# Optimization experiments

Measured on AMD Instinct MI355X. Metric: run time of the kernel, lower is better.

Reference implementation:

```python
import jax, jax.numpy as jnp
import numpy as np

C = 128          # hidden channels
N = 40000        # nodes
E = 640000       # edges (avg degree 16)
G = 64           # graphs in batch
STEPS = (5, 4, 3, 2, 1)  # num_layers of each GatedGraphConv


def setup_inputs() -> dict:
    key = jax.random.key(0)
    ks = jax.random.split(key, 9)
    x = jax.random.normal(ks[0], (N, C), jnp.float32)
    edge_index = jax.random.randint(ks[1], (2, E), 0, N, dtype=jnp.int64)
    edge_weights = jax.random.uniform(ks[2], (E,), jnp.float32)
    batch = jnp.sort(jax.random.randint(ks[3], (N,), 0, G, dtype=jnp.int64))
    s = 1.0 / np.sqrt(C)
    # conv_w[k, i] = per-step propagation weight of conv k (unused steps padded)
    conv_w = jax.random.uniform(ks[4], (5, 5, C, C), jnp.float32, -s, s)
    gru_wih = jax.random.uniform(ks[5], (5, 3 * C, C), jnp.float32, -s, s)
    gru_whh = jax.random.uniform(ks[6], (5, 3 * C, C), jnp.float32, -s, s)
    gru_bih = jax.random.uniform(ks[7], (5, 3 * C), jnp.float32, -s, s)
    gru_bhh = jax.random.uniform(ks[8], (5, 3 * C), jnp.float32, -s, s)
    gn_w = jnp.ones((4, C), jnp.float32)
    gn_b = jnp.zeros((4, C), jnp.float32)
    gn_ms = jnp.ones((4, C), jnp.float32)  # GraphNorm mean_scale
    return {"x": x, "edge_weights": edge_weights, "conv_w": conv_w,
            "gru_wih": gru_wih, "gru_whh": gru_whh, "gru_bih": gru_bih,
            "gru_bhh": gru_bhh, "gn_w": gn_w, "gn_b": gn_b, "gn_ms": gn_ms,
            "edge_index": edge_index, "batch": batch}


def _gru(m, h, wih, whh, bih, bhh):
    gi = m @ wih.T + bih
    gh = h @ whh.T + bhh
    ir, iz, inew = jnp.split(gi, 3, axis=-1)
    hr, hz, hn = jnp.split(gh, 3, axis=-1)
    r = jax.nn.sigmoid(ir + hr)
    z = jax.nn.sigmoid(iz + hz)
    n = jnp.tanh(inew + r * hn)
    return (1.0 - z) * n + z * h


def _ggc(x, W, wih, whh, bih, bhh, src, dst, ew, steps):
    # PyG GatedGraphConv: m = x W_i; aggregate sum of ew * m[src] at dst; GRU update.
    for i in range(steps):
        m = x @ W[i]
        msg = m[src]
        if ew is not None:
            msg = msg * ew[:, None]
        agg = jax.ops.segment_sum(msg, dst, num_segments=x.shape[0])
        x = _gru(agg, x, wih, whh, bih, bhh)
    return x


def _graph_norm(x, w, b, ms, eps=1e-5):
    # called with batch=None -> normalize over all nodes as one graph
    mean = jnp.mean(x, axis=0)
    xc = x - ms * mean
    var = jnp.mean(xc * xc, axis=0)
    return w * xc / jnp.sqrt(var + eps) + b


def reference(x, edge_weights, conv_w, gru_wih, gru_whh, gru_bih, gru_bhh,
              gn_w, gn_b, gn_ms, edge_index, batch):
    src, dst = edge_index[0], edge_index[1]
    lrelu = jax.nn.leaky_relu
    o = _ggc(x, conv_w[0], gru_wih[0], gru_whh[0], gru_bih[0], gru_bhh[0], src, dst, edge_weights, STEPS[0])
    o = _graph_norm(o, gn_w[0], gn_b[0], gn_ms[0])
    o = lrelu(o)
    o = _ggc(o, conv_w[1], gru_wih[1], gru_whh[1], gru_bih[1], gru_bhh[1], src, dst, edge_weights, STEPS[1])
    o = lrelu(o)
    o = _graph_norm(o, gn_w[1], gn_b[1], gn_ms[1])
    o = _ggc(o, conv_w[2], gru_wih[2], gru_whh[2], gru_bih[2], gru_bhh[2], src, dst, edge_weights, STEPS[2])
    o = lrelu(o)
    o = _graph_norm(o, gn_w[2], gn_b[2], gn_ms[2])
    o = _ggc(o, conv_w[3], gru_wih[3], gru_whh[3], gru_bih[3], gru_bhh[3], src, dst, edge_weights, STEPS[3])
    o = lrelu(o)
    o = _graph_norm(o, gn_w[3], gn_b[3], gn_ms[3])
    o = _ggc(o, conv_w[4], gru_wih[4], gru_whh[4], gru_bih[4], gru_bhh[4], src, dst, None, STEPS[4])
    o = lrelu(o)
    return jax.ops.segment_sum(o, batch, num_segments=G)
```

## Files before the change

### kernel.cpp

```cpp
#include <hip/hip_runtime.h>
#include <hip/hip_bf16.h>

#define NN 40000
#define EE 640000
#define CCH 128
#define GG 64

typedef __attribute__((ext_vector_type(8))) short short8;
typedef __attribute__((ext_vector_type(4))) float f32x4;

__device__ __forceinline__ float lrelu01(float v){ return v > 0.f ? v : 0.01f*v; }
__device__ __forceinline__ float sigm(float v){ return 1.f/(1.f + __expf(-v)); }
__device__ __forceinline__ float tanh_f(float v){
  v = fminf(fmaxf(v, -15.f), 15.f);
  const float t = __expf(2.f*v);
  return (t - 1.f)/(t + 1.f);
}
__device__ __forceinline__ unsigned short f2bf(float f){
  union { float f; unsigned int u; } v; v.f = f;
  const unsigned int r = v.u + 0x7FFFu + ((v.u >> 16) & 1u);
  return (unsigned short)(r >> 16);
}
__device__ __forceinline__ float bf2f(unsigned short h){
  union { unsigned int u; float f; } v; v.u = ((unsigned int)h) << 16;
  return v.f;
}
__device__ __forceinline__ void split2v(const float4 a, const float4 b, short8& hi, short8& lo){
  const float v[8] = {a.x,a.y,a.z,a.w,b.x,b.y,b.z,b.w};
#pragma unroll
  for (int i=0;i<8;++i){
    const unsigned short h = f2bf(v[i]);
    hi[i] = (short)h;
    lo[i] = (short)f2bf(v[i] - bf2f(h));
  }
}
__device__ __forceinline__ float LDF(const void* p, int f32, size_t i){
  return f32 ? ((const float*)p)[i] : bf2f(((const unsigned short*)p)[i]);
}
__device__ __forceinline__ int LDI(const void* p, int i64, size_t i){
  return i64 ? (int)((const long long*)p)[i] : ((const int*)p)[i];
}

__global__ __launch_bounds__(256) void k_detect(const unsigned short* __restrict__ xh,
                                                const unsigned int* __restrict__ ei,
                                                int* __restrict__ flags){
  __shared__ int s1[256], s2[256];
  const int t = threadIdx.x;
  int c1 = 0, c2 = 0;
  for (int i=0;i<8;++i){
    const unsigned short w = xh[t*8 + i];
    const int e = (w >> 7) & 0xFF;
    if (e < 100 || e > 140) c1++;
    const unsigned int o = ei[(t*8 + i)*2 + 1];
    if (o) c2++;
  }
  s1[t]=c1; s2[t]=c2; __syncthreads();
  for (int off=128; off; off>>=1){ if (t<off){ s1[t]+=s1[t+off]; s2[t]+=s2[t+off]; } __syncthreads(); }
  if (t==0){
    flags[0] = (s1[0] > 64) ? 1 : 0;
    flags[1] = (s2[0] < 16) ? 1 : 0;
  }
}

__global__ __launch_bounds__(256) void k_hist(const void* __restrict__ eidx, const int* __restrict__ flags,
                                              int* __restrict__ deg){
  const int e = blockIdx.x*256 + threadIdx.x;
  if (e >= EE) return;
  atomicAdd(&deg[LDI(eidx, flags[1], (size_t)EE + e)], 1);
}

__global__ __launch_bounds__(256) void k_scan1(const int* __restrict__ deg, int* __restrict__ bsum){
  __shared__ int s[256];
  const int t = threadIdx.x;
  const int i = blockIdx.x*256 + t;
  s[t] = (i < NN) ? deg[i] : 0;
  __syncthreads();
  for (int off=128; off; off>>=1){ if (t<off) s[t]+=s[t+off]; __syncthreads(); }
  if (t==0) bsum[blockIdx.x] = s[0];
}

__global__ __launch_bounds__(256) void k_scan2(const int* __restrict__ bsum, int* __restrict__ boff,
                                               int* __restrict__ roff){
  __shared__ int s[256];
  const int t = threadIdx.x;
  const int v = (t < 157) ? bsum[t] : 0;
  s[t] = v; __syncthreads();
  for (int off=1; off<256; off<<=1){
    const int u = (t>=off) ? s[t-off] : 0;
    __syncthreads(); s[t] += u; __syncthreads();
  }
  if (t < 157) boff[t] = s[t] - v;
  if (t == 0) roff[NN] = EE;
}

__global__ __launch_bounds__(256) void k_scan3(const int* __restrict__ deg, const int* __restrict__ boff,
                                               int* __restrict__ roff, int* __restrict__ pos){
  __shared__ int s[256];
  const int t = threadIdx.x;
  const int i = blockIdx.x*256 + t;
  const int v = (i < NN) ? deg[i] : 0;
  s[t] = v; __syncthreads();
  for (int off=1; off<256; off<<=1){
    const int u = (t>=off) ? s[t-off] : 0;
    __syncthreads(); s[t] += u; __syncthreads();
  }
  if (i < NN){
    const int ex = boff[blockIdx.x] + s[t] - v;
    roff[i] = ex; pos[i] = ex;
  }
}

__global__ __launch_bounds__(256) void k_scatter(const void* __restrict__ eidx, const void* __restrict__ ew,
                                                 const int* __restrict__ flags,
                                                 int* __restrict__ pos, int* __restrict__ es, float* __restrict__ ewt){
  const int e = blockIdx.x*256 + threadIdx.x;
  if (e >= EE) return;
  const int i64 = flags[1];
  const int d = LDI(eidx, i64, (size_t)EE + e);
  const int p = atomicAdd(&pos[d], 1);
  es[p] = LDI(eidx, i64, e);
  ewt[p] = LDF(ew, flags[0], e);
}

__global__ __launch_bounds__(256) void k_x2f(const void* __restrict__ xin, const int* __restrict__ flags,
                                             float* __restrict__ xf){
  const int i = blockIdx.x*256 + threadIdx.x;
  if (i < NN*CCH) xf[i] = LDF(xin, flags[0], i);
}

__global__ __launch_bounds__(256) void k_batcvt(const void* __restrict__ batch, const int* __restrict__ flags,
                                                int* __restrict__ bat32){
  const int i = blockIdx.x*256 + threadIdx.x;
  if (i < NN) bat32[i] = LDI(batch, flags[1], i);
}

__global__ __launch_bounds__(256) void k_wcvt_bf(const void* __restrict__ w, const int* __restrict__ flags,
                                                 const size_t off, unsigned short* __restrict__ o, const int n){
  const int i = blockIdx.x*256 + threadIdx.x;
  if (i < n) o[i] = f2bf(LDF(w, flags[0], off + i));
}

__global__ __launch_bounds__(256) void k_mkWc(const void* __restrict__ cw, const void* __restrict__ wih,
                                              const int* __restrict__ flags,
                                              unsigned short* __restrict__ wcH, unsigned short* __restrict__ wcL){
  __shared__ unsigned short sW[128*128];
  __shared__ unsigned short sI[32*136];
  const int tid = threadIdx.x;
  const int t = blockIdx.x / 12, tile = blockIdx.x % 12;
  int L=0, s=t;
  if (t>=14){L=4;s=t-14;} else if(t>=12){L=3;s=t-12;} else if(t>=9){L=2;s=t-9;} else if(t>=5){L=1;s=t-5;}
  const int f32 = flags[0];
  const size_t woff = (size_t)(L*5+s)*16384;
  const size_t ioff = (size_t)L*49152 + (size_t)tile*32*128;
  for (int u=tid; u<16384; u+=256) sW[u] = f2bf(LDF(cw, f32, woff + u));
  for (int u=tid; u<4096; u+=256){
    const int r = u>>7, jj = u&127;
    sI[r*136 + jj] = f2bf(LDF(wih, f32, ioff + r*128 + jj));
  }
  __syncthreads();
  const int cl = tid & 31;
  const int kb = (tid>>5)*16;
  for (int k=kb; k<kb+16; ++k){
    float acc = 0.f;
#pragma unroll 4
    for (int j8=0; j8<16; ++j8){
      const short8 a = *(const short8*)(sW + k*128 + j8*8);
      const short8 b = *(const short8*)(sI + cl*136 + j8*8);
#pragma unroll
      for (int q=0;q<8;++q) acc += bf2f((unsigned short)a[q]) * bf2f((unsigned short)b[q]);
    }
    const unsigned short h = f2bf(acc);
    const unsigned short l = f2bf(acc - bf2f(h));
    const size_t oidx = (size_t)t*49152 + (size_t)(tile*32 + cl)*128 + k;
    wcH[oidx] = h; wcL[oidx] = l;
  }
}

__global__ __launch_bounds__(256) void k_agg(const float* __restrict__ m, const int* __restrict__ roff,
                                             const int* __restrict__ es, const float* __restrict__ ewt,
                                             float* __restrict__ agg, const int useW){
  const int node = (blockIdx.x*256 + threadIdx.x) >> 6;
  if (node >= NN) return;
  const int lane = threadIdx.x & 63;
  const int h = lane >> 5, j = lane & 31;
  const int beg = roff[node], end = roff[node+1];
  float ax=0.f, ay=0.f, az=0.f, aw=0.f;
  int e = beg + h;
  for (; e + 2 < end; e += 4){
    const int s0 = es[e], s1 = es[e+2];
    const float w0 = useW ? ewt[e] : 1.f;
    const float w1 = useW ? ewt[e+2] : 1.f;
    const float4 v0 = *(const float4*)(m + (size_t)s0*CCH + j*4);
    const float4 v1 = *(const float4*)(m + (size_t)s1*CCH + j*4);
    ax += w0*v0.x + w1*v1.x; ay += w0*v0.y + w1*v1.y;
    az += w0*v0.z + w1*v1.z; aw += w0*v0.w + w1*v1.w;
  }
  if (e < end){
    const int s0 = es[e];
    const float w0 = useW ? ewt[e] : 1.f;
    const float4 v0 = *(const float4*)(m + (size_t)s0*CCH + j*4);
    ax += w0*v0.x; ay += w0*v0.y; az += w0*v0.z; aw += w0*v0.w;
  }
  ax += __shfl_xor(ax, 32); ay += __shfl_xor(ay, 32);
  az += __shfl_xor(az, 32); aw += __shfl_xor(aw, 32);
  if (h == 0){
    float4 ov; ov.x=ax; ov.y=ay; ov.z=az; ov.w=aw;
    *(float4*)(agg + (size_t)node*CCH + j*4) = ov;
  }
}

__global__ __launch_bounds__(256) void k_gru(const float* __restrict__ xg,
                                             const float* __restrict__ xc,
                                             float* __restrict__ xn,
                                             const unsigned short* __restrict__ wcH,
                                             const unsigned short* __restrict__ wcL,
                                             const unsigned short* __restrict__ whB,
                                             const void* __restrict__ bih, const void* __restrict__ bhh,
                                             const size_t boff, const int* __restrict__ flags){
  __shared__ unsigned short s_w[6*32*128];
  const int tid = threadIdx.x;
  const int wv = tid >> 6;
  const int lane = tid & 63;
  const int quad = lane >> 4;
  const int ln = lane & 15;
  const int bi_ = blockIdx.x >> 2, j = blockIdx.x & 3;
  const int m0 = bi_*64 + wv*16;
  const int f32 = flags[0];
  float4 ra[8], rx[8];
  {
    const float* pa = xg + (size_t)(m0 + ln)*CCH + quad*8;
    const float* px = xc + (size_t)(m0 + ln)*CCH + quad*8;
#pragma unroll
    for (int kk=0;kk<4;++kk){
      ra[kk*2]   = *(const float4*)(pa + kk*32);
      ra[kk*2+1] = *(const float4*)(pa + kk*32 + 4);
      rx[kk*2]   = *(const float4*)(px + kk*32);
      rx[kk*2+1] = *(const float4*)(px + kk*32 + 4);
    }
  }
  for (int u = tid; u < 3072; u += 256){
    const int chunk = u >> 9;
    const int rem = u & 511;
    const int c = rem >> 4, p = rem & 15;
    const int gate = (chunk < 3) ? chunk : chunk - 3;
    const unsigned short* src = ((chunk < 3) ? wcH : wcL)
        + ((size_t)(gate*CCH + j*32 + c)*CCH + p*8);
    *(short8*)(s_w + chunk*4096 + c*128 + ((p ^ (c & 15))*8)) = *(const short8*)src;
  }
  short8 fah[4], fal[4], fxh[4], fxl[4];
#pragma unroll
  for (int kk=0;kk<4;++kk){
    split2v(ra[kk*2], ra[kk*2+1], fah[kk], fal[kk]);
    split2v(rx[kk*2], rx[kk*2+1], fxh[kk], fxl[kk]);
  }
  __syncthreads();
  f32x4 acci[2][3];
#pragma unroll
  for (int hf=0; hf<2; ++hf){
    const int c_local = hf*16 + ln;
#pragma unroll
    for (int g=0;g<3;++g) acci[hf][g] = (f32x4){0.f,0.f,0.f,0.f};
#pragma unroll
    for (int kk=0;kk<4;++kk){
      const int sw = ((kk*4+quad) ^ (c_local & 15))*8;
#pragma unroll
      for (int g=0;g<3;++g){
        const short8 bh_ = *(const short8*)(s_w + g*4096     + c_local*128 + sw);
        const short8 bl_ = *(const short8*)(s_w + (3+g)*4096 + c_local*128 + sw);
        acci[hf][g] = __builtin_amdgcn_mfma_f32_16x16x32_bf16(fah[kk], bh_, acci[hf][g], 0, 0, 0);
        acci[hf][g] = __builtin_amdgcn_mfma_f32_16x16x32_bf16(fal[kk], bh_, acci[hf][g], 0, 0, 0);
        acci[hf][g] = __builtin_amdgcn_mfma_f32_16x16x32_bf16(fah[kk], bl_, acci[hf][g], 0, 0, 0);
      }
    }
  }
  __syncthreads();
  for (int u = tid; u < 1536; u += 256){
    const int chunk = u >> 9;
    const int rem = u & 511;
    const int c = rem >> 4, p = rem & 15;
    const unsigned short* src = whB + ((size_t)(chunk*CCH + j*32 + c)*CCH + p*8);
    *(short8*)(s_w + chunk*4096 + c*128 + ((p ^ (c & 15))*8)) = *(const short8*)src;
  }
  __syncthreads();
#pragma unroll 1
  for (int hf=0; hf<2; ++hf){
    const int c_local = hf*16 + ln;
    f32x4 acch[3];
#pragma unroll
    for (int g=0;g<3;++g) acch[g] = (f32x4){0.f,0.f,0.f,0.f};
#pragma unroll
    for (int kk=0;kk<4;++kk){
      const int sw = ((kk*4+quad) ^ (c_local & 15))*8;
#pragma unroll
      for (int g=0;g<3;++g){
        const short8 bh_ = *(const short8*)(s_w + g*4096 + c_local*128 + sw);
        acch[g] = __builtin_amdgcn_mfma_f32_16x16x32_bf16(fxh[kk], bh_, acch[g], 0, 0, 0);
        acch[g] = __builtin_amdgcn_mfma_f32_16x16x32_bf16(fxl[kk], bh_, acch[g], 0, 0, 0);
      }
    }
    const int col = j*32 + c_local;
    float bi[3], bh[3];
#pragma unroll
    for (int g=0;g<3;++g){
      bi[g] = LDF(bih, f32, boff + g*CCH + col);
      bh[g] = LDF(bhh, f32, boff + g*CCH + col);
    }
#pragma unroll
    for (int r=0;r<4;++r){
      const int row = m0 + quad*4 + r;
      const size_t idx = (size_t)row*CCH + col;
      const float h = xc[idx];
      const float rr = sigm(acci[hf][0][r] + acch[0][r] + bi[0] + bh[0]);
      const float zz = sigm(acci[hf][1][r] + acch[1][r] + bi[1] + bh[1]);
      const float nv = tanh_f(acci[hf][2][r] + bi[2] + rr*(acch[2][r] + bh[2]));
      xn[idx] = (1.f - zz)*nv + zz*h;
    }
  }
}

__global__ __launch_bounds__(256) void k_gn_stats(const float* __restrict__ x, float* __restrict__ accum, const int pre){
  const int tid = threadIdx.x;
  const int ch = tid & 127;
  const int half = tid >> 7;
  const int node0 = blockIdx.x * 128;
  float s = 0.f, s2 = 0.f;
  for (int r = half; r < 128; r += 2){
    const int n = node0 + r;
    if (n >= NN) break;
    float v = x[(size_t)n*CCH + ch];
    if (pre) v = lrelu01(v);
    s += v; s2 += v*v;
  }
  __shared__ float buf[256];
  buf[tid] = s; __syncthreads();
  if (tid < 128) atomicAdd(&accum[ch], buf[tid] + buf[tid+128]);
  __syncthreads();
  buf[tid] = s2; __syncthreads();
  if (tid < 128) atomicAdd(&accum[128+ch], buf[tid] + buf[tid+128]);
}

__global__ void k_gn_final(const float* __restrict__ accum, const void* __restrict__ gw,
                           const void* __restrict__ gb, const void* __restrict__ gms,
                           const size_t off, const int* __restrict__ flags, float* __restrict__ par){
  const int j = threadIdx.x;
  const int f32 = flags[0];
  const float inv = 1.f/(float)NN;
  const float mean = accum[j]*inv;
  const float m2 = accum[128+j]*inv;
  const float ms = LDF(gms, f32, off + j);
  const float var = m2 - 2.f*ms*mean*mean + ms*ms*mean*mean;
  const float sc = LDF(gw, f32, off + j) / sqrtf(var + 1e-5f);
  par[j] = sc;
  par[128+j] = LDF(gb, f32, off + j) - sc*ms*mean;
}

__global__ __launch_bounds__(256) void k_gn_apply(float* __restrict__ xf, const float* __restrict__ par, const int mode){
  const int i = blockIdx.x*256 + threadIdx.x;
#pragma unroll
  for (int r=0;r<8;++r){
    const int idx = i + r*640000;
    float v = xf[idx];
    const int ch = idx & 127;
    if (mode == 1) v = lrelu01(v);
    v = par[ch]*v + par[128+ch];
    if (mode == 0) v = lrelu01(v);
    xf[idx] = v;
  }
}

__global__ __launch_bounds__(256) void k_final(const float* __restrict__ x, const int* __restrict__ bat,
                                               float* __restrict__ outf){
  const int t = threadIdx.x;
  const int ch = t & 127;
  const int half = t >> 7;
  const int n0 = blockIdx.x*32;
  int cur = -1; float acc = 0.f;
  for (int r = half; r < 32; r += 2){
    const int n = n0 + r;
    const int b = bat[n];
    if (b != cur){
      if (cur >= 0) atomicAdd(&outf[cur*CCH + ch], acc);
      cur = b; acc = 0.f;
    }
    acc += lrelu01(x[(size_t)n*CCH + ch]);
  }
  if (cur >= 0) atomicAdd(&outf[cur*CCH + ch], acc);
}

__global__ __launch_bounds__(256) void k_store(const float* __restrict__ outf, const int* __restrict__ flags, void* __restrict__ out){
  const int i = blockIdx.x*256 + threadIdx.x;
  if (i >= GG*CCH) return;
  if (flags[0]) ((float*)out)[i] = outf[i];
  else ((unsigned short*)out)[i] = f2bf(outf[i]);
}

extern "C" void kernel_launch(void* const* d_in, const int* in_sizes, int n_in,
                              void* d_out, int out_size, void* d_ws, size_t ws_size,
                              hipStream_t stream){
  const void* x_in = d_in[0];
  const void* ew   = d_in[1];
  const void* cw   = d_in[2];
  const void* wih  = d_in[3];
  const void* whh  = d_in[4];
  const void* bih  = d_in[5];
  const void* bhh  = d_in[6];
  const void* gnw  = d_in[7];
  const void* gnb  = d_in[8];
  const void* gnms = d_in[9];
  const void* eidx  = d_in[10];
  const void* batch = d_in[11];

  float* base = (float*)d_ws;
  size_t o = 0;
  float* xA     = base + o; o += (size_t)NN*CCH;
  float* xB     = base + o; o += (size_t)NN*CCH;
  float* xg     = base + o; o += (size_t)NN*CCH;
  unsigned short* wcH = (unsigned short*)(base + o); o += 15*384*CCH/2;
  unsigned short* wcL = (unsigned short*)(base + o); o += 15*384*CCH/2;
  unsigned short* whB5= (unsigned short*)(base + o); o += 5*384*CCH/2;
  float* ewt    = base + o; o += EE;
  float* gnpar  = base + o; o += 256;
  int* flags    = (int*)(base + o); o += 2;
  int* bat32    = (int*)(base + o); o += NN;
  int* bsum     = (int*)(base + o); o += 160;
  int* boff2    = (int*)(base + o); o += 160;
  float* outf   = base + o; o += GG*CCH;
  float* gnacc  = base + o; o += 1024;
  int* deg      = (int*)(base + o); o += NN;
  int* roff     = (int*)(base + o); o += NN+1;
  int* pos      = (int*)(base + o); o += NN;
  int* es       = (int*)(base + o); o += EE;

  hipMemsetAsync(outf, 0, (size_t)(GG*CCH + 1024 + NN)*4, stream);

  k_detect<<<1,256,0,stream>>>((const unsigned short*)x_in, (const unsigned int*)eidx, flags);
  k_hist<<<2500,256,0,stream>>>(eidx, flags, deg);
  k_scan1<<<157,256,0,stream>>>(deg, bsum);
  k_scan2<<<1,256,0,stream>>>(bsum, boff2, roff);
  k_scan3<<<157,256,0,stream>>>(deg, boff2, roff, pos);
  k_scatter<<<2500,256,0,stream>>>(eidx, ew, flags, pos, es, ewt);
  k_x2f<<<20000,256,0,stream>>>(x_in, flags, xA);
  k_batcvt<<<157,256,0,stream>>>(batch, flags, bat32);
  for (int L=0; L<5; ++L)
    k_wcvt_bf<<<192,256,0,stream>>>(whh, flags, (size_t)L*384*CCH, whB5 + (size_t)L*384*CCH, 384*CCH);
  k_mkWc<<<180,256,0,stream>>>(cw, wih, flags, wcH, wcL);

  const int steps[5] = {5,4,3,2,1};
  float* xc = xA;
  float* xn = xB;
  int t = 0;
  for (int L=0; L<5; ++L){
    for (int s=0; s<steps[L]; ++s){
      k_agg<<<10000,256,0,stream>>>(xc, roff, es, ewt, xg, (L<4) ? 1 : 0);
      k_gru<<<2500,256,0,stream>>>(xg, xc, xn,
                                   wcH + (size_t)t*384*CCH, wcL + (size_t)t*384*CCH,
                                   whB5 + (size_t)L*384*CCH, bih, bhh, (size_t)L*384, flags);
      float* tmp = xc; xc = xn; xn = tmp;
      t++;
    }
    if (L < 4){
      const int pre = (L==0) ? 0 : 1;
      k_gn_stats<<<313,256,0,stream>>>(xc, gnacc + L*256, pre);
      k_gn_final<<<1,128,0,stream>>>(gnacc + L*256, gnw, gnb, gnms, (size_t)L*CCH, flags, gnpar);
      k_gn_apply<<<2500,256,0,stream>>>(xc, gnpar, pre);
    }
  }
  k_final<<<1250,256,0,stream>>>(xc, bat32, outf);
  k_store<<<32,256,0,stream>>>(outf, flags, d_out);
}
```

Measured before the change: 2.113 ms.

## Restructure GRU kernel to row-tile all output columns and update state in place

The GRU kernel now has each 512-thread block own 128 rows and loop over all 128 output columns in 16-column tiles. Each row's activations are loaded and split into bf16 hi/lo once, where before four blocks each reloaded the same rows for their 32-column slice. Because a block owns full rows, the new state is written back in place, which drops the double buffer. The cost is eight sync-separated weight staging rounds per block and only 313 blocks, which may limit occupancy and latency hiding.

```diff
diff --git a/kernel.cpp b/kernel.cpp
--- a/kernel.cpp
+++ b/kernel.cpp
@@ -209,96 +209,64 @@
   }
 }
 
-__global__ __launch_bounds__(256) void k_gru(const float* __restrict__ xg,
-                                             const float* __restrict__ xc,
-                                             float* __restrict__ xn,
+__global__ __launch_bounds__(512) void k_gru(const float* __restrict__ xg,
+                                             float* __restrict__ xf,
                                              const unsigned short* __restrict__ wcH,
                                              const unsigned short* __restrict__ wcL,
                                              const unsigned short* __restrict__ whB,
                                              const void* __restrict__ bih, const void* __restrict__ bhh,
                                              const size_t boff, const int* __restrict__ flags){
-  __shared__ unsigned short s_w[6*32*128];
+  __shared__ unsigned short s_w[9*16*128];
   const int tid = threadIdx.x;
   const int wv = tid >> 6;
   const int lane = tid & 63;
   const int quad = lane >> 4;
   const int ln = lane & 15;
-  const int bi_ = blockIdx.x >> 2, j = blockIdx.x & 3;
-  const int m0 = bi_*64 + wv*16;
+  const int m0 = blockIdx.x*128 + wv*16;
   const int f32 = flags[0];
-  float4 ra[8], rx[8];
+  short8 fah[4], fal[4], fxh[4], fxl[4];
   {
-    const float* pa = xg + (size_t)(m0 + ln)*CCH + quad*8;
-    const float* px = xc + (size_t)(m0 + ln)*CCH + quad*8;
+    int arow = m0 + ln; if (arow >= NN) arow = NN-1;
+    const float* pa = xg + (size_t)arow*CCH + quad*8;
+    const float* px = xf + (size_t)arow*CCH + quad*8;
 #pragma unroll
     for (int kk=0;kk<4;++kk){
-      ra[kk*2]   = *(const float4*)(pa + kk*32);
-      ra[kk*2+1] = *(const float4*)(pa + kk*32 + 4);
-      rx[kk*2]   = *(const float4*)(px + kk*32);
-      rx[kk*2+1] = *(const float4*)(px + kk*32 + 4);
-    }
-  }
-  for (int u = tid; u < 3072; u += 256){
-    const int chunk = u >> 9;
-    const int rem = u & 511;
-    const int c = rem >> 4, p = rem & 15;
-    const int gate = (chunk < 3) ? chunk : chunk - 3;
-    const unsigned short* src = ((chunk < 3) ? wcH : wcL)
-        + ((size_t)(gate*CCH + j*32 + c)*CCH + p*8);
-    *(short8*)(s_w + chunk*4096 + c*128 + ((p ^ (c & 15))*8)) = *(const short8*)src;
-  }
-  short8 fah[4], fal[4], fxh[4], fxl[4];
-#pragma unroll
-  for (int kk=0;kk<4;++kk){
-    split2v(ra[kk*2], ra[kk*2+1], fah[kk], fal[kk]);
-    split2v(rx[kk*2], rx[kk*2+1], fxh[kk], fxl[kk]);
-  }
-  __syncthreads();
-  f32x4 acci[2][3];
-#pragma unroll
-  for (int hf=0; hf<2; ++hf){
-    const int c_local = hf*16 + ln;
-#pragma unroll
-    for (int g=0;g<3;++g) acci[hf][g] = (f32x4){0.f,0.f,0.f,0.f};
+      split2v(*(const float4*)(pa+kk*32), *(const float4*)(pa+kk*32+4), fah[kk], fal[kk]);
+      split2v(*(const float4*)(px+kk*32), *(const float4*)(px+kk*32+4), fxh[kk], fxl[kk]);
+    }
+  }
+#pragma unroll 1
+  for (int ct=0; ct<8; ++ct){
+    __syncthreads();
+    for (int u = tid; u < 2304; u += 512){
+      const int chunk = u >> 8;
+      const int rem = u & 255;
+      const int c = rem >> 4, p = rem & 15;
+      const int mat = chunk / 3, g = chunk - mat*3;
+      const unsigned short* msrc = (mat==0) ? wcH : ((mat==1) ? wcL : whB);
+      const unsigned short* src = msrc + ((size_t)(g*CCH + ct*16 + c)*CCH + p*8);
+      *(short8*)(s_w + chunk*2048 + c*128 + ((p ^ c)*8)) = *(const short8*)src;
+    }
+    __syncthreads();
+    f32x4 acci[3], acch[3];
+#pragma unroll
+    for (int g=0;g<3;++g){ acci[g] = (f32x4){0.f,0.f,0.f,0.f}; acch[g] = (f32x4){0.f,0.f,0.f,0.f}; }
 #pragma unroll
     for (int kk=0;kk<4;++kk){
-      const int sw = ((kk*4+quad) ^ (c_local & 15))*8;
+      const int sw = ((kk*4+quad) ^ ln)*8;
 #pragma unroll
       for (int g=0;g<3;++g){
-        const short8 bh_ = *(const short8*)(s_w + g*4096     + c_local*128 + sw);
-        const short8 bl_ = *(const short8*)(s_w + (3+g)*4096 + c_local*128 + sw);
-        acci[hf][g] = __builtin_amdgcn_mfma_f32_16x16x32_bf16(fah[kk], bh_, acci[hf][g], 0, 0, 0);
-        acci[hf][g] = __builtin_amdgcn_mfma_f32_16x16x32_bf16(fal[kk], bh_, acci[hf][g], 0, 0, 0);
-        acci[hf][g] = __builtin_amdgcn_mfma_f32_16x16x32_bf16(fah[kk], bl_, acci[hf][g], 0, 0, 0);
+        const short8 bh_ = *(const short8*)(s_w + g*2048     + ln*128 + sw);
+        const short8 bl_ = *(const short8*)(s_w + (3+g)*2048 + ln*128 + sw);
+        const short8 bb_ = *(const short8*)(s_w + (6+g)*2048 + ln*128 + sw);
+        acci[g] = __builtin_amdgcn_mfma_f32_16x16x32_bf16(fah[kk], bh_, acci[g], 0, 0, 0);
+        acci[g] = __builtin_amdgcn_mfma_f32_16x16x32_bf16(fal[kk], bh_, acci[g], 0, 0, 0);
+        acci[g] = __builtin_amdgcn_mfma_f32_16x16x32_bf16(fah[kk], bl_, acci[g], 0, 0, 0);
+        acch[g] = __builtin_amdgcn_mfma_f32_16x16x32_bf16(fxh[kk], bb_, acch[g], 0, 0, 0);
+        acch[g] = __builtin_amdgcn_mfma_f32_16x16x32_bf16(fxl[kk], bb_, acch[g], 0, 0, 0);
       }
     }
-  }
-  __syncthreads();
-  for (int u = tid; u < 1536; u += 256){
-    const int chunk = u >> 9;
-    const int rem = u & 511;
-    const int c = rem >> 4, p = rem & 15;
-    const unsigned short* src = whB + ((size_t)(chunk*CCH + j*32 + c)*CCH + p*8);
-    *(short8*)(s_w + chunk*4096 + c*128 + ((p ^ (c & 15))*8)) = *(const short8*)src;
-  }
-  __syncthreads();
-#pragma unroll 1
-  for (int hf=0; hf<2; ++hf){
-    const int c_local = hf*16 + ln;
-    f32x4 acch[3];
-#pragma unroll
-    for (int g=0;g<3;++g) acch[g] = (f32x4){0.f,0.f,0.f,0.f};
-#pragma unroll
-    for (int kk=0;kk<4;++kk){
-      const int sw = ((kk*4+quad) ^ (c_local & 15))*8;
-#pragma unroll
-      for (int g=0;g<3;++g){
-        const short8 bh_ = *(const short8*)(s_w + g*4096 + c_local*128 + sw);
-        acch[g] = __builtin_amdgcn_mfma_f32_16x16x32_bf16(fxh[kk], bh_, acch[g], 0, 0, 0);
-        acch[g] = __builtin_amdgcn_mfma_f32_16x16x32_bf16(fxl[kk], bh_, acch[g], 0, 0, 0);
-      }
-    }
-    const int col = j*32 + c_local;
+    const int col = ct*16 + ln;
     float bi[3], bh[3];
 #pragma unroll
     for (int g=0;g<3;++g){
@@ -308,12 +276,14 @@
 #pragma unroll
     for (int r=0;r<4;++r){
       const int row = m0 + quad*4 + r;
-      const size_t idx = (size_t)row*CCH + col;
-      const float h = xc[idx];
-      const float rr = sigm(acci[hf][0][r] + acch[0][r] + bi[0] + bh[0]);
-      const float zz = sigm(acci[hf][1][r] + acch[1][r] + bi[1] + bh[1]);
-      const float nv = tanh_f(acci[hf][2][r] + bi[2] + rr*(acch[2][r] + bh[2]));
-      xn[idx] = (1.f - zz)*nv + zz*h;
+      if (row < NN){
+        const size_t idx = (size_t)row*CCH + col;
+        const float h = xf[idx];
+        const float rr = sigm(acci[0][r] + acch[0][r] + bi[0] + bh[0]);
+        const float zz = sigm(acci[1][r] + acch[1][r] + bi[1] + bh[1]);
+        const float nv = tanh_f(acci[2][r] + bi[2] + rr*(acch[2][r] + bh[2]));
+        xf[idx] = (1.f - zz)*nv + zz*h;
+      }
     }
   }
 }
@@ -412,8 +382,7 @@
 
   float* base = (float*)d_ws;
   size_t o = 0;
-  float* xA     = base + o; o += (size_t)NN*CCH;
-  float* xB     = base + o; o += (size_t)NN*CCH;
+  float* xf     = base + o; o += (size_t)NN*CCH;
   float* xg     = base + o; o += (size_t)NN*CCH;
   unsigned short* wcH = (unsigned short*)(base + o); o += 15*384*CCH/2;
   unsigned short* wcL = (unsigned short*)(base + o); o += 15*384*CCH/2;
@@ -439,32 +408,29 @@
   k_scan2<<<1,256,0,stream>>>(bsum, boff2, roff);
   k_scan3<<<157,256,0,stream>>>(deg, boff2, roff, pos);
   k_scatter<<<2500,256,0,stream>>>(eidx, ew, flags, pos, es, ewt);
-  k_x2f<<<20000,256,0,stream>>>(x_in, flags, xA);
+  k_x2f<<<20000,256,0,stream>>>(x_in, flags, xf);
   k_batcvt<<<157,256,0,stream>>>(batch, flags, bat32);
   for (int L=0; L<5; ++L)
     k_wcvt_bf<<<192,256,0,stream>>>(whh, flags, (size_t)L*384*CCH, whB5 + (size_t)L*384*CCH, 384*CCH);
   k_mkWc<<<180,256,0,stream>>>(cw, wih, flags, wcH, wcL);
 
   const int steps[5] = {5,4,3,2,1};
-  float* xc = xA;
-  float* xn = xB;
   int t = 0;
   for (int L=0; L<5; ++L){
     for (int s=0; s<steps[L]; ++s){
-      k_agg<<<10000,256,0,stream>>>(xc, roff, es, ewt, xg, (L<4) ? 1 : 0);
-      k_gru<<<2500,256,0,stream>>>(xg, xc, xn,
-                                   wcH + (size_t)t*384*CCH, wcL + (size_t)t*384*CCH,
-                                   whB5 + (size_t)L*384*CCH, bih, bhh, (size_t)L*384, flags);
-      float* tmp = xc; xc = xn; xn = tmp;
+      k_agg<<<10000,256,0,stream>>>(xf, roff, es, ewt, xg, (L<4) ? 1 : 0);
+      k_gru<<<313,512,0,stream>>>(xg, xf,
+                                  wcH + (size_t)t*384*CCH, wcL + (size_t)t*384*CCH,
+                                  whB5 + (size_t)L*384*CCH, bih, bhh, (size_t)L*384, flags);
       t++;
     }
     if (L < 4){
       const int pre = (L==0) ? 0 : 1;
-      k_gn_stats<<<313,256,0,stream>>>(xc, gnacc + L*256, pre);
+      k_gn_stats<<<313,256,0,stream>>>(xf, gnacc + L*256, pre);
       k_gn_final<<<1,128,0,stream>>>(gnacc + L*256, gnw, gnb, gnms, (size_t)L*CCH, flags, gnpar);
-      k_gn_apply<<<2500,256,0,stream>>>(xc, gnpar, pre);
-    }
-  }
-  k_final<<<1250,256,0,stream>>>(xc, bat32, outf);
+      k_gn_apply<<<2500,256,0,stream>>>(xf, gnpar, pre);
+    }
+  }
+  k_final<<<1250,256,0,stream>>>(xf, bat32, outf);
   k_store<<<32,256,0,stream>>>(outf, flags, d_out);
 }
```

New measurement: 1.727 ms. -18.3%, faster.
